# Performance work log

Measured on AMD Instinct MI355X. Metric: run time of the kernel, lower is better.

Reference implementation:

```python
import jax, jax.numpy as jnp
import numpy as np

WINDOW = 5
SIGMA = 4.0
KSIZE = 2 * int(4.0 * SIGMA + 0.5) + 1  # 33, matches torchvision GaussianBlur setup

H1, W1, B, N, C = 56, 56, 16, 32, 512
PAD = WINDOW - 1


def _gauss_kernel():
    x = jnp.arange(KSIZE, dtype=jnp.float32) - (KSIZE - 1) / 2.0
    k = jnp.exp(-0.5 * (x / SIGMA) ** 2)
    return k / jnp.sum(k)


def _blur(img):
    # separable Gaussian blur with reflect padding (torchvision GaussianBlur default)
    k = _gauss_kernel()
    p = KSIZE // 2
    x = jnp.pad(img, ((0, 0), (0, 0), (p, p), (p, p)), mode='reflect')
    dn = ('NCHW', 'OIHW', 'NCHW')
    x = jax.lax.conv_general_dilated(x, k.reshape(1, 1, KSIZE, 1), (1, 1), 'VALID', dimension_numbers=dn)
    x = jax.lax.conv_general_dilated(x, k.reshape(1, 1, 1, KSIZE), (1, 1), 'VALID', dimension_numbers=dn)
    return x


def _forward(embeddings, memory_bank, out_h, out_w):
    H, W, Bb, Cc = embeddings.shape
    x_norm = jnp.sum(embeddings * embeddings, axis=-1, keepdims=True)  # H W B 1
    best = None
    for d1 in range(WINDOW):
        for d2 in range(WINDOW):
            y = memory_bank[d1:H + d1, d2:W + d2]            # H W N C (shifted slice)
            y_norm = jnp.sum(y * y, axis=-1)                  # H W N
            cross = jnp.einsum('hwbc,hwnc->hwbn', embeddings, y)
            dsq = jnp.maximum(x_norm - 2.0 * cross + y_norm[:, :, None, :], 0.0)
            dmin = jnp.sqrt(jnp.min(dsq, axis=-1))            # H W B
            best = dmin if best is None else jnp.minimum(best, dmin)
    pix = jnp.transpose(best, (2, 0, 1))[:, None, :, :]        # B 1 H W
    img = jnp.max(pix, axis=(1, 2, 3))                         # B
    pix = jax.image.resize(pix, (Bb, 1, out_h, out_w), method='linear')  # align_corners=False bilinear
    return img, _blur(pix)


def setup_inputs() -> dict:
    key = jax.random.key(0)
    k1, k2 = jax.random.split(key)
    embeddings = jax.random.normal(k1, (H1, W1, B, C), dtype=jnp.float32)
    memory_bank = jax.random.normal(k2, (H1 + PAD, W1 + PAD, N, C), dtype=jnp.float32)
    return {'embeddings': embeddings, 'memory_bank': memory_bank, 'out_h': 224, 'out_w': 224}


def reference(embeddings, memory_bank, out_h, out_w):
    return _forward(embeddings, memory_bank, out_h, out_w)
```

## Files before the change

kernel.cpp:

```cpp
#include <hip/hip_runtime.h>
#include <math.h>

#define H1 56
#define W1 56
#define BB 16
#define NN 32
#define CC 512
#define MH 60
#define MW 60
#define OH 224
#define OW 224

typedef __bf16 bf16x8 __attribute__((ext_vector_type(8)));
typedef float floatx4 __attribute__((ext_vector_type(4)));

#define MBH_OFF    0
#define F_YN_OFF   29491200
#define F_BEST_OFF 29606400
#define F_TMP1_OFF 29656576
#define F_TOTAL_FLOATS 29857280ull

#define S_XN_OFF   0
#define S_YN_OFF   50176
#define S_BEST_OFF 165376
#define S_TMP1_OFF 215552

#define GLOAD_LDS16(g, l) __builtin_amdgcn_global_load_lds( \
    (const __attribute__((address_space(1))) unsigned int*)(g), \
    (__attribute__((address_space(3))) unsigned int*)(l), 16, 0, 0)

__global__ void cvt_norm_kernel(const float* __restrict__ src, __bf16* __restrict__ dsth,
                                float* __restrict__ norm, int nvec) {
    int wid  = (int)((blockIdx.x * blockDim.x + threadIdx.x) >> 6);
    int lane = threadIdx.x & 63;
    if (wid >= nvec) return;
    const float* p = src + (size_t)wid * CC + lane * 8;
    floatx4 a = *(const floatx4*)p;
    floatx4 b = *(const floatx4*)(p + 4);
    if (dsth) {
        bf16x8 v;
        v[0] = (__bf16)a.x; v[1] = (__bf16)a.y; v[2] = (__bf16)a.z; v[3] = (__bf16)a.w;
        v[4] = (__bf16)b.x; v[5] = (__bf16)b.y; v[6] = (__bf16)b.z; v[7] = (__bf16)b.w;
        *(bf16x8*)(dsth + (size_t)wid * CC + lane * 8) = v;
    }
    float s = a.x*a.x + a.y*a.y + a.z*a.z + a.w*a.w
            + b.x*b.x + b.y*b.y + b.z*b.z + b.w*b.w;
    s += __shfl_xor(s, 32, 64);
    s += __shfl_xor(s, 16, 64);
    s += __shfl_xor(s, 8, 64);
    s += __shfl_xor(s, 4, 64);
    s += __shfl_xor(s, 2, 64);
    s += __shfl_xor(s, 1, 64);
    if (lane == 0) norm[wid] = s;
}

#define BSTRIDE 520
#define HROWS 16

__global__ __launch_bounds__(256, 2) void dist_kernel_bf16(
        const float* __restrict__ emb, const __bf16* __restrict__ mbh,
        const float* __restrict__ ynorm, float* __restrict__ best) {
    __shared__ __bf16 Bs[2][HROWS * BSTRIDE];
    __shared__ float Ys[6 * 8 * NN];

    int bx0  = blockIdx.x;
    int bx   = (bx0 & 7) * 49 + (bx0 >> 3);
    int h0   = (bx / 14) * 2;
    int w0   = (bx % 14) * 4;
    int tid  = threadIdx.x;
    int wave = tid >> 6;
    int lane = tid & 63;
    int nrow = lane & 15;
    int seg  = lane >> 4;
    int w    = w0 + wave;

    bf16x8 afragA[16], afragB[16];
    float snA = 0.f, snB = 0.f;
    const float* apA = emb + ((size_t)(h0 * W1 + w) * BB + nrow) * CC + seg * 8;
    const float* apB = apA + (size_t)W1 * BB * CC;
#pragma unroll
    for (int kk = 0; kk < 16; kk++) {
        floatx4 a0 = *(const floatx4*)(apA + kk * 32);
        floatx4 a1 = *(const floatx4*)(apA + kk * 32 + 4);
        floatx4 b0 = *(const floatx4*)(apB + kk * 32);
        floatx4 b1 = *(const floatx4*)(apB + kk * 32 + 4);
        bf16x8 va, vb;
        va[0] = (__bf16)a0.x; va[1] = (__bf16)a0.y; va[2] = (__bf16)a0.z; va[3] = (__bf16)a0.w;
        va[4] = (__bf16)a1.x; va[5] = (__bf16)a1.y; va[6] = (__bf16)a1.z; va[7] = (__bf16)a1.w;
        vb[0] = (__bf16)b0.x; vb[1] = (__bf16)b0.y; vb[2] = (__bf16)b0.z; vb[3] = (__bf16)b0.w;
        vb[4] = (__bf16)b1.x; vb[5] = (__bf16)b1.y; vb[6] = (__bf16)b1.z; vb[7] = (__bf16)b1.w;
        afragA[kk] = va; afragB[kk] = vb;
        snA += a0.x*a0.x + a0.y*a0.y + a0.z*a0.z + a0.w*a0.w
             + a1.x*a1.x + a1.y*a1.y + a1.z*a1.z + a1.w*a1.w;
        snB += b0.x*b0.x + b0.y*b0.y + b0.z*b0.z + b0.w*b0.w
             + b1.x*b1.x + b1.y*b1.y + b1.z*b1.z + b1.w*b1.w;
    }
    snA += __shfl_xor(snA, 16, 64); snA += __shfl_xor(snA, 32, 64);
    snB += __shfl_xor(snB, 16, 64); snB += __shfl_xor(snB, 32, 64);
    floatx4 xnA, xnB;
#pragma unroll
    for (int r = 0; r < 4; r++) {
        xnA[r] = __shfl(snA, seg * 4 + r, 64);
        xnB[r] = __shfl(snB, seg * 4 + r, 64);
    }

    for (int idx = tid; idx < 6 * 8 * NN; idx += 256) {
        int row = idx >> 8;
        int c   = idx & 255;
        Ys[idx] = ynorm[((size_t)((h0 + row) * MW + w0)) * NN + c];
    }

    float bvA[4] = {1e30f, 1e30f, 1e30f, 1e30f};
    float bvB[4] = {1e30f, 1e30f, 1e30f, 1e30f};

    auto stage = [&](int t, int buf) {
        int p  = t >> 1;
        int hh = t & 1;
        int rr = p >> 3;
        int j  = p & 7;
        const __bf16* bp = mbh + ((size_t)((h0 + rr) * MW + (w0 + j)) * NN + hh * HROWS) * CC;
#pragma unroll
        for (int tt = 0; tt < 4; tt++) {
            int n = wave * 4 + tt;
            GLOAD_LDS16(bp + (size_t)n * CC + lane * 8, &Bs[buf][n * BSTRIDE]);
        }
    };

    stage(0, 0);
    __syncthreads();

    for (int t = 0; t < 96; t++) {
        int cur = t & 1;
        if (t + 1 < 96) stage(t + 1, cur ^ 1);

        int p  = t >> 1;
        int hh = t & 1;
        int rr = p >> 3;
        int j  = p & 7;
        int d2 = j - wave;
        if (d2 >= 0 && d2 < 5) {
            const __bf16* Bc = &Bs[cur][0];
            float yn = Ys[(rr * 8 + j) * NN + hh * 16 + nrow];
            floatx4 cA = {0,0,0,0}, cB = {0,0,0,0};
#pragma unroll
            for (int kk = 0; kk < 16; kk++) {
                bf16x8 b = *(const bf16x8*)(Bc + nrow * BSTRIDE + kk * 32 + seg * 8);
                cA = __builtin_amdgcn_mfma_f32_16x16x32_bf16(afragA[kk], b, cA, 0, 0, 0);
                cB = __builtin_amdgcn_mfma_f32_16x16x32_bf16(afragB[kk], b, cB, 0, 0, 0);
            }
            bool va = (rr < 5);
            bool vb = (rr >= 1);
#pragma unroll
            for (int r = 0; r < 4; r++) {
                float dA = fmaxf(xnA[r] - 2.f * cA[r] + yn, 0.f);
                float dB = fmaxf(xnB[r] - 2.f * cB[r] + yn, 0.f);
                bvA[r] = fminf(bvA[r], va ? dA : 1e30f);
                bvB[r] = fminf(bvB[r], vb ? dB : 1e30f);
            }
        }
        __syncthreads();
    }

#pragma unroll
    for (int r = 0; r < 4; r++) {
        float v = bvA[r];
        v = fminf(v, __shfl_xor(v, 1, 64));
        v = fminf(v, __shfl_xor(v, 2, 64));
        v = fminf(v, __shfl_xor(v, 4, 64));
        v = fminf(v, __shfl_xor(v, 8, 64));
        bvA[r] = v;
        float u = bvB[r];
        u = fminf(u, __shfl_xor(u, 1, 64));
        u = fminf(u, __shfl_xor(u, 2, 64));
        u = fminf(u, __shfl_xor(u, 4, 64));
        u = fminf(u, __shfl_xor(u, 8, 64));
        bvB[r] = u;
    }
    if ((lane & 15) == 0) {
        int posA = h0 * W1 + w;
        int posB = (h0 + 1) * W1 + w;
#pragma unroll
        for (int r = 0; r < 4; r++) {
            int b = seg * 4 + r;
            best[(size_t)b * (H1 * W1) + posA] = sqrtf(bvA[r]);
            best[(size_t)b * (H1 * W1) + posB] = sqrtf(bvB[r]);
        }
    }
}

__global__ __launch_bounds__(256) void dist_kernel_f32(
        const float* __restrict__ emb, const float* __restrict__ mb,
        const float* __restrict__ xnorm, const float* __restrict__ ynorm,
        float* __restrict__ best) {
    __shared__ __bf16 Bs[NN * BSTRIDE];
    int bx   = blockIdx.x;
    int h    = bx / 14;
    int w0   = (bx % 14) * 4;
    int tid  = threadIdx.x;
    int wave = tid >> 6;
    int lane = tid & 63;
    int nrow = lane & 15;
    int seg  = lane >> 4;
    int w    = w0 + wave;

    bf16x8 afrag[16];
    const float* ap = emb + ((size_t)(h * W1 + w) * BB + nrow) * CC + seg * 8;
#pragma unroll
    for (int kk = 0; kk < 16; kk++) {
        floatx4 f0 = *(const floatx4*)(ap + kk * 32);
        floatx4 f1 = *(const floatx4*)(ap + kk * 32 + 4);
        bf16x8 v;
        v[0] = (__bf16)f0.x; v[1] = (__bf16)f0.y; v[2] = (__bf16)f0.z; v[3] = (__bf16)f0.w;
        v[4] = (__bf16)f1.x; v[5] = (__bf16)f1.y; v[6] = (__bf16)f1.z; v[7] = (__bf16)f1.w;
        afrag[kk] = v;
    }
    floatx4 xn = *(const floatx4*)(xnorm + (size_t)(h * W1 + w) * BB + seg * 4);
    float bestv[4] = {1e30f, 1e30f, 1e30f, 1e30f};

    for (int d1 = 0; d1 < 5; d1++) {
        int mr = h + d1;
        for (int j = 0; j < 8; j++) {
            int mc = w0 + j;
            const float* bp = mb + (size_t)(mr * MW + mc) * NN * CC;
            __syncthreads();
#pragma unroll
            for (int t = 0; t < 8; t++) {
                int c0 = t * 256 + tid;
                int n  = c0 >> 6;
                int ks = (c0 & 63) << 3;
                floatx4 f0 = *(const floatx4*)(bp + n * CC + ks);
                floatx4 f1 = *(const floatx4*)(bp + n * CC + ks + 4);
                bf16x8 v;
                v[0] = (__bf16)f0.x; v[1] = (__bf16)f0.y; v[2] = (__bf16)f0.z; v[3] = (__bf16)f0.w;
                v[4] = (__bf16)f1.x; v[5] = (__bf16)f1.y; v[6] = (__bf16)f1.z; v[7] = (__bf16)f1.w;
                *(bf16x8*)(&Bs[n * BSTRIDE + ks]) = v;
            }
            __syncthreads();

            int d2 = j - wave;
            if (d2 >= 0 && d2 < 5) {
                float yn0 = ynorm[(size_t)(mr * MW + mc) * NN + nrow];
                float yn1 = ynorm[(size_t)(mr * MW + mc) * NN + nrow + 16];
                floatx4 acc0 = {0,0,0,0};
                floatx4 acc1 = {0,0,0,0};
#pragma unroll
                for (int kk = 0; kk < 16; kk++) {
                    bf16x8 b0 = *(const bf16x8*)(&Bs[nrow * BSTRIDE + kk * 32 + seg * 8]);
                    bf16x8 b1 = *(const bf16x8*)(&Bs[(nrow + 16) * BSTRIDE + kk * 32 + seg * 8]);
                    acc0 = __builtin_amdgcn_mfma_f32_16x16x32_bf16(afrag[kk], b0, acc0, 0, 0, 0);
                    acc1 = __builtin_amdgcn_mfma_f32_16x16x32_bf16(afrag[kk], b1, acc1, 0, 0, 0);
                }
#pragma unroll
                for (int r = 0; r < 4; r++) {
                    float d0  = fmaxf(xn[r] - 2.f * acc0[r] + yn0, 0.f);
                    float d1v = fmaxf(xn[r] - 2.f * acc1[r] + yn1, 0.f);
                    bestv[r] = fminf(bestv[r], fminf(d0, d1v));
                }
            }
        }
    }
#pragma unroll
    for (int r = 0; r < 4; r++) {
        float v = bestv[r];
        v = fminf(v, __shfl_xor(v, 1, 64));
        v = fminf(v, __shfl_xor(v, 2, 64));
        v = fminf(v, __shfl_xor(v, 4, 64));
        v = fminf(v, __shfl_xor(v, 8, 64));
        bestv[r] = v;
    }
    if ((lane & 15) == 0) {
        int pos = h * W1 + w;
#pragma unroll
        for (int r = 0; r < 4; r++) {
            int b = seg * 4 + r;
            best[(size_t)b * (H1 * W1) + pos] = sqrtf(bestv[r]);
        }
    }
}

__global__ void max_kernel(const float* __restrict__ best, float* __restrict__ out) {
    __shared__ float red[256];
    int b = blockIdx.x;
    float m = 0.f;
    for (int i = threadIdx.x; i < H1 * W1; i += 256)
        m = fmaxf(m, best[(size_t)b * (H1 * W1) + i]);
    red[threadIdx.x] = m;
    __syncthreads();
    for (int s = 128; s > 0; s >>= 1) {
        if (threadIdx.x < s) red[threadIdx.x] = fmaxf(red[threadIdx.x], red[threadIdx.x + s]);
        __syncthreads();
    }
    if (threadIdx.x == 0) out[b] = red[0];
}

struct GaussK { float k[33]; };

__device__ __forceinline__ int refl(int i, int n) {
    i = (i < 0) ? -i : i;
    i = (i > n - 1) ? 2 * (n - 1) - i : i;
    return i;
}

__global__ void vblur_kernel(const float* __restrict__ best, float* __restrict__ tmp1, GaussK g) {
    int idx = blockIdx.x * 256 + threadIdx.x;
    int lx = idx % W1;
    int y  = (idx / W1) % OH;
    int b  = idx / (W1 * OH);
    const float* p = best + (size_t)b * (H1 * W1);
    float acc = 0.f;
#pragma unroll
    for (int u = 0; u < 33; u++) {
        int z  = refl(y - 16 + u, OH);
        int rz = z & 3;
        float t = 0.125f + 0.25f * (float)((rz + 2) & 3);
        int lo = (z >> 2) + ((rz < 2) ? -1 : 0);
        int hi = min(lo + 1, H1 - 1);
        lo = max(lo, 0);
        acc += g.k[u] * ((1.f - t) * p[lo * W1 + lx] + t * p[hi * W1 + lx]);
    }
    tmp1[idx] = acc;
}

__global__ void hblur_kernel(const float* __restrict__ tmp1, float* __restrict__ dst, GaussK g) {
    int idx = blockIdx.x * 256 + threadIdx.x;
    int x = idx % OW;
    int y = (idx / OW) % OH;
    int b = idx / (OW * OH);
    const float* p = tmp1 + ((size_t)b * OH + y) * W1;
    float acc = 0.f;
#pragma unroll
    for (int u = 0; u < 33; u++) {
        int z  = refl(x - 16 + u, OW);
        int rz = z & 3;
        float t = 0.125f + 0.25f * (float)((rz + 2) & 3);
        int lo = (z >> 2) + ((rz < 2) ? -1 : 0);
        int hi = min(lo + 1, W1 - 1);
        lo = max(lo, 0);
        acc += g.k[u] * ((1.f - t) * p[lo] + t * p[hi]);
    }
    dst[idx] = acc;
}

extern "C" void kernel_launch(void* const* d_in, const int* in_sizes, int n_in,
                              void* d_out, int out_size, void* d_ws, size_t ws_size,
                              hipStream_t stream) {
    const float* emb = (const float*)d_in[0];
    const float* mbp = (const float*)d_in[1];
    float* ws  = (float*)d_ws;
    float* out = (float*)d_out;

    bool big = ws_size >= F_TOTAL_FLOATS * 4ull;

    float* best;
    float* tmp1;

    if (big) {
        __bf16* mbh  = (__bf16*)(ws + MBH_OFF);
        float* ynorm = ws + F_YN_OFF;
        best = ws + F_BEST_OFF;
        tmp1 = ws + F_TMP1_OFF;
        cvt_norm_kernel<<<(MH * MW * NN) / 4, 256, 0, stream>>>(mbp, mbh, ynorm, MH * MW * NN);
        dist_kernel_bf16<<<28 * 14, 256, 0, stream>>>(emb, mbh, ynorm, best);
    } else {
        float* xnorm = ws + S_XN_OFF;
        float* ynorm = ws + S_YN_OFF;
        best = ws + S_BEST_OFF;
        tmp1 = ws + S_TMP1_OFF;
        cvt_norm_kernel<<<(H1 * W1 * BB) / 4, 256, 0, stream>>>(emb, nullptr, xnorm, H1 * W1 * BB);
        cvt_norm_kernel<<<(MH * MW * NN) / 4, 256, 0, stream>>>(mbp, nullptr, ynorm, MH * MW * NN);
        dist_kernel_f32<<<H1 * 14, 256, 0, stream>>>(emb, mbp, xnorm, ynorm, best);
    }

    max_kernel<<<BB, 256, 0, stream>>>(best, out);

    GaussK g;
    {
        double wsum = 0.0, wd[33];
        for (int u = 0; u < 33; u++) {
            double xk = (u - 16) / 4.0;
            wd[u] = exp(-0.5 * xk * xk);
            wsum += wd[u];
        }
        for (int u = 0; u < 33; u++) g.k[u] = (float)(wd[u] / wsum);
    }
    vblur_kernel<<<(BB * OH * W1) / 256, 256, 0, stream>>>(best, tmp1, g);
    hblur_kernel<<<(BB * OH * OW) / 256, 256, 0, stream>>>(tmp1, out + 16, g);
}
```

Baseline: 537.9 us.

## Split bf16 distance kernel over memory-bank row halves with second grid dimension

```diff
diff --git a/kernel.cpp b/kernel.cpp
--- a/kernel.cpp
+++ b/kernel.cpp
@@ -14,11 +14,12 @@
 typedef __bf16 bf16x8 __attribute__((ext_vector_type(8)));
 typedef float floatx4 __attribute__((ext_vector_type(4)));
 
-#define MBH_OFF    0
-#define F_YN_OFF   29491200
-#define F_BEST_OFF 29606400
-#define F_TMP1_OFF 29656576
-#define F_TOTAL_FLOATS 29857280ull
+#define MBH_OFF     0
+#define F_YN_OFF    29491200
+#define F_BEST0_OFF 29606400
+#define F_BEST1_OFF 29656576
+#define F_TMP1_OFF  29706752
+#define F_TOTAL_FLOATS 29907456ull
 
 #define S_XN_OFF   0
 #define S_YN_OFF   50176
@@ -59,12 +60,15 @@
 
 __global__ __launch_bounds__(256, 2) void dist_kernel_bf16(
         const float* __restrict__ emb, const __bf16* __restrict__ mbh,
-        const float* __restrict__ ynorm, float* __restrict__ best) {
+        const float* __restrict__ ynorm, float* __restrict__ best0,
+        float* __restrict__ best1) {
     __shared__ __bf16 Bs[2][HROWS * BSTRIDE];
-    __shared__ float Ys[6 * 8 * NN];
+    __shared__ float Ys[3 * 8 * NN];
 
     int bx0  = blockIdx.x;
     int bx   = (bx0 & 7) * 49 + (bx0 >> 3);
+    int z    = blockIdx.y;
+    float* bestz = z ? best1 : best0;
     int h0   = (bx / 14) * 2;
     int w0   = (bx % 14) * 4;
     int tid  = threadIdx.x;
@@ -104,21 +108,22 @@
         xnB[r] = __shfl(snB, seg * 4 + r, 64);
     }
 
-    for (int idx = tid; idx < 6 * 8 * NN; idx += 256) {
+    for (int idx = tid; idx < 3 * 8 * NN; idx += 256) {
         int row = idx >> 8;
         int c   = idx & 255;
-        Ys[idx] = ynorm[((size_t)((h0 + row) * MW + w0)) * NN + c];
+        Ys[idx] = ynorm[((size_t)((h0 + 3 * z + row) * MW + w0)) * NN + c];
     }
 
     float bvA[4] = {1e30f, 1e30f, 1e30f, 1e30f};
     float bvB[4] = {1e30f, 1e30f, 1e30f, 1e30f};
 
     auto stage = [&](int t, int buf) {
-        int p  = t >> 1;
-        int hh = t & 1;
-        int rr = p >> 3;
-        int j  = p & 7;
-        const __bf16* bp = mbh + ((size_t)((h0 + rr) * MW + (w0 + j)) * NN + hh * HROWS) * CC;
+        int p   = t >> 1;
+        int hh  = t & 1;
+        int rrL = p >> 3;
+        int j   = p & 7;
+        const __bf16* bp = mbh + ((size_t)((h0 + 3 * z + rrL) * MW + (w0 + j)) * NN
+                                  + hh * HROWS) * CC;
 #pragma unroll
         for (int tt = 0; tt < 4; tt++) {
             int n = wave * 4 + tt;
@@ -129,18 +134,19 @@
     stage(0, 0);
     __syncthreads();
 
-    for (int t = 0; t < 96; t++) {
+    for (int t = 0; t < 48; t++) {
         int cur = t & 1;
-        if (t + 1 < 96) stage(t + 1, cur ^ 1);
-
-        int p  = t >> 1;
-        int hh = t & 1;
-        int rr = p >> 3;
-        int j  = p & 7;
-        int d2 = j - wave;
+        if (t + 1 < 48) stage(t + 1, cur ^ 1);
+
+        int p   = t >> 1;
+        int hh  = t & 1;
+        int rrL = p >> 3;
+        int j   = p & 7;
+        int rr  = 3 * z + rrL;
+        int d2  = j - wave;
         if (d2 >= 0 && d2 < 5) {
             const __bf16* Bc = &Bs[cur][0];
-            float yn = Ys[(rr * 8 + j) * NN + hh * 16 + nrow];
+            float yn = Ys[(rrL * 8 + j) * NN + hh * 16 + nrow];
             floatx4 cA = {0,0,0,0}, cB = {0,0,0,0};
 #pragma unroll
             for (int kk = 0; kk < 16; kk++) {
@@ -182,8 +188,8 @@
 #pragma unroll
         for (int r = 0; r < 4; r++) {
             int b = seg * 4 + r;
-            best[(size_t)b * (H1 * W1) + posA] = sqrtf(bvA[r]);
-            best[(size_t)b * (H1 * W1) + posB] = sqrtf(bvB[r]);
+            bestz[(size_t)b * (H1 * W1) + posA] = sqrtf(bvA[r]);
+            bestz[(size_t)b * (H1 * W1) + posB] = sqrtf(bvB[r]);
         }
     }
 }
@@ -278,12 +284,17 @@
     }
 }
 
-__global__ void max_kernel(const float* __restrict__ best, float* __restrict__ out) {
+__global__ void max_kernel(float* __restrict__ best0, const float* __restrict__ best1,
+                           float* __restrict__ out) {
     __shared__ float red[256];
     int b = blockIdx.x;
     float m = 0.f;
-    for (int i = threadIdx.x; i < H1 * W1; i += 256)
-        m = fmaxf(m, best[(size_t)b * (H1 * W1) + i]);
+    for (int i = threadIdx.x; i < H1 * W1; i += 256) {
+        size_t idx = (size_t)b * (H1 * W1) + i;
+        float v = fminf(best0[idx], best1[idx]);
+        best0[idx] = v;
+        m = fmaxf(m, v);
+    }
     red[threadIdx.x] = m;
     __syncthreads();
     for (int s = 128; s > 0; s >>= 1) {
@@ -351,27 +362,30 @@
 
     bool big = ws_size >= F_TOTAL_FLOATS * 4ull;
 
-    float* best;
+    float* best0;
+    float* best1;
     float* tmp1;
 
     if (big) {
         __bf16* mbh  = (__bf16*)(ws + MBH_OFF);
         float* ynorm = ws + F_YN_OFF;
-        best = ws + F_BEST_OFF;
-        tmp1 = ws + F_TMP1_OFF;
+        best0 = ws + F_BEST0_OFF;
+        best1 = ws + F_BEST1_OFF;
+        tmp1  = ws + F_TMP1_OFF;
         cvt_norm_kernel<<<(MH * MW * NN) / 4, 256, 0, stream>>>(mbp, mbh, ynorm, MH * MW * NN);
-        dist_kernel_bf16<<<28 * 14, 256, 0, stream>>>(emb, mbh, ynorm, best);
+        dist_kernel_bf16<<<dim3(28 * 14, 2), 256, 0, stream>>>(emb, mbh, ynorm, best0, best1);
     } else {
         float* xnorm = ws + S_XN_OFF;
         float* ynorm = ws + S_YN_OFF;
-        best = ws + S_BEST_OFF;
-        tmp1 = ws + S_TMP1_OFF;
+        best0 = ws + S_BEST_OFF;
+        best1 = best0;
+        tmp1  = ws + S_TMP1_OFF;
         cvt_norm_kernel<<<(H1 * W1 * BB) / 4, 256, 0, stream>>>(emb, nullptr, xnorm, H1 * W1 * BB);
         cvt_norm_kernel<<<(MH * MW * NN) / 4, 256, 0, stream>>>(mbp, nullptr, ynorm, MH * MW * NN);
-        dist_kernel_f32<<<H1 * 14, 256, 0, stream>>>(emb, mbp, xnorm, ynorm, best);
-    }
-
-    max_kernel<<<BB, 256, 0, stream>>>(best, out);
+        dist_kernel_f32<<<H1 * 14, 256, 0, stream>>>(emb, mbp, xnorm, ynorm, best0);
+    }
+
+    max_kernel<<<BB, 256, 0, stream>>>(best0, best1, out);
 
     GaussK g;
     {
@@ -383,6 +397,6 @@
         }
         for (int u = 0; u < 33; u++) g.k[u] = (float)(wd[u] / wsum);
     }
-    vblur_kernel<<<(BB * OH * W1) / 256, 256, 0, stream>>>(best, tmp1, g);
+    vblur_kernel<<<(BB * OH * W1) / 256, 256, 0, stream>>>(best0, tmp1, g);
     hblur_kernel<<<(BB * OH * OW) / 256, 256, 0, stream>>>(tmp1, out + 16, g);
 }
```

New measurement: 546.0 us. About the same (+1.5%).
